# Kernel tuning notes

Hardware: AMD Instinct MI355X
Metric: run time of the kernel (lower is better)

Reference implementation:

```python
import jax, jax.numpy as jnp
import numpy as np

B, L, C, H, DK, MAXREL = 4, 1024, 768, 12, 64, 7
NEG = -2.0 ** 15  # masked_fill value


def _rel_pos_table(L, m):
    # abs distance, compressed logarithmically beyond m, clipped to [0, 2m]
    i = jnp.arange(L, dtype=jnp.float32)
    d = jnp.abs(i[:, None] - i[None, :])
    comp = m + jnp.log2(jnp.maximum(d - m, 1.0))
    d = jnp.where(d > m, comp, d)
    return jnp.clip(d, 0, 2 * m).astype(jnp.int32)  # [L, L]


def setup_inputs() -> dict:
    key = jax.random.key(0)
    ks = jax.random.split(key, 16)
    s = 0.02
    return {
        "qx": jax.random.normal(ks[0], (B, L, C), jnp.float32),
        "kx": jax.random.normal(ks[1], (B, L, C), jnp.float32),
        "vx": jax.random.normal(ks[2], (B, L, C), jnp.float32),
        "WQ_w": jax.random.normal(ks[3], (C, H * DK), jnp.float32) * s,
        "WQ_b": jnp.zeros((H * DK,), jnp.float32),
        "WK_w": jax.random.normal(ks[4], (C, H * DK), jnp.float32) * s,
        "WK_b": jnp.zeros((H * DK,), jnp.float32),
        "WV_w": jax.random.normal(ks[5], (C, H * DK), jnp.float32) * s,
        "WV_b": jnp.zeros((H * DK,), jnp.float32),
        "WO_w": jax.random.normal(ks[6], (H * DK, C), jnp.float32) * s,
        "WO_b": jnp.zeros((C,), jnp.float32),
        "embK": jax.random.normal(ks[7], (2 * MAXREL + 1, H), jnp.float32),
        "embB": jax.random.normal(ks[8], (2 * MAXREL + 1, H), jnp.float32) * s,
        "preScores": jax.random.normal(ks[9], (B, H, L, L), jnp.float32) * 0.1,
        "maskPAD": jnp.ones((B, L, L), jnp.int32),
    }


def reference(qx, kx, vx, WQ_w, WQ_b, WK_w, WK_b, WV_w, WV_b, WO_w, WO_b,
              embK, embB, preScores, maskPAD):
    q = (qx @ WQ_w + WQ_b).reshape(B, L, H, DK).transpose(0, 2, 1, 3)  # [B,H,L,dk]
    k = (kx @ WK_w + WK_b).reshape(B, L, H, DK).transpose(0, 2, 1, 3)
    v = (vx @ WV_w + WV_b).reshape(B, L, H, DK).transpose(0, 2, 1, 3)

    scores = jnp.einsum('bhid,bhjd->bhij', q, k) / np.sqrt(DK).astype(np.float32)

    tab = _rel_pos_table(L, MAXREL)                 # [L, L] int
    relK = jnp.transpose(embK[tab], (2, 1, 0))      # [H, L, L] (torch transpose(0,-1))
    relB = jnp.transpose(embB[tab], (2, 1, 0))
    scores = scores * relK[None] + relB[None]

    scores = scores + preScores
    scores = jnp.where((maskPAD == 0)[:, None, :, :], jnp.float32(NEG), scores)

    alpha = jax.nn.softmax(scores, axis=-1)         # dropout is identity in eval
    z = jnp.einsum('bhij,bhjd->bhid', alpha, v)     # [B,H,L,dk]
    z = z.transpose(0, 2, 1, 3).reshape(B, L, H * DK)
    z = z @ WO_w + WO_b
    return (z, scores)
```

## Files before the change

### kernel.cpp

```cpp
#include <hip/hip_runtime.h>
#include <stdint.h>


typedef __attribute__((ext_vector_type(4))) float f32x4;
typedef __attribute__((ext_vector_type(4))) int   i32x4;
typedef __attribute__((ext_vector_type(8))) short short8;
typedef __attribute__((ext_vector_type(4))) unsigned int u32x4;
typedef __attribute__((ext_vector_type(2))) unsigned int u32x2;

__device__ __forceinline__ unsigned short f2bf(float f) {
  unsigned int u = __float_as_uint(f);
  u += 0x7fffu + ((u >> 16) & 1u);
  return (unsigned short)(u >> 16);
}

__global__ __launch_bounds__(256) void conv_x_kernel(
    const float* __restrict__ qx, const float* __restrict__ kx,
    const float* __restrict__ vx, unsigned short* __restrict__ out) {
  int v = blockIdx.x * 256 + threadIdx.x;
  int mat = v / 786432;
  int r = v - mat * 786432;
  const float* src = (mat == 0) ? qx : (mat == 1) ? kx : vx;
  f32x4 x = ((const f32x4*)src)[r];
  union { unsigned short s[4]; u32x2 u; } o;
  o.s[0] = f2bf(x[0]); o.s[1] = f2bf(x[1]); o.s[2] = f2bf(x[2]); o.s[3] = f2bf(x[3]);
  ((u32x2*)out)[v] = o.u;
}

__global__ __launch_bounds__(256) void conv_w_kernel(
    const float* __restrict__ w0, const float* __restrict__ w1,
    const float* __restrict__ w2, const float* __restrict__ w3,
    unsigned short* __restrict__ out) {
  __shared__ float T[64][65];
  int bx = blockIdx.x;
  int mat = bx / 144; int t2 = bx - mat * 144;
  int kt = t2 / 12, nt = t2 - kt * 12;
  int k0 = kt * 64, n0 = nt * 64;
  const float* W = (mat == 0) ? w0 : (mat == 1) ? w1 : (mat == 2) ? w2 : w3;
  unsigned short* WT = out + (size_t)mat * 589824;
  int t = threadIdx.x;
  int lr = t >> 4;
  int lc = (t & 15) * 4;
#pragma unroll
  for (int p = 0; p < 4; p++) {
    int row = p * 16 + lr;
    f32x4 x = *(const f32x4*)&W[(size_t)(k0 + row) * 768 + n0 + lc];
    T[lc + 0][row] = x[0]; T[lc + 1][row] = x[1];
    T[lc + 2][row] = x[2]; T[lc + 3][row] = x[3];
  }
  __syncthreads();
#pragma unroll
  for (int p = 0; p < 4; p++) {
    int row = p * 16 + lr;
    union { unsigned short s[4]; u32x2 u; } o;
    o.s[0] = f2bf(T[row][lc + 0]); o.s[1] = f2bf(T[row][lc + 1]);
    o.s[2] = f2bf(T[row][lc + 2]); o.s[3] = f2bf(T[row][lc + 3]);
    *(u32x2*)&WT[(size_t)(n0 + row) * 768 + k0 + lc] = o.u;
  }
}

__global__ __launch_bounds__(256) void qkv_gemm_kernel(
    const unsigned short* __restrict__ xbf, const unsigned short* __restrict__ wt,
    const float* __restrict__ bq, const float* __restrict__ bk, const float* __restrict__ bv,
    unsigned short* __restrict__ qo, unsigned short* __restrict__ ko,
    unsigned short* __restrict__ vto) {
  __shared__ unsigned short As[128 * 72];
  __shared__ unsigned short Bs[128 * 72];
  int bx = blockIdx.x;
  int mat = bx / 192; int rem = bx - mat * 192;
  int mt = rem / 6, nt = rem - mt * 6;
  int m0 = mt * 128, n0 = nt * 128;
  const unsigned short* A = xbf + (size_t)mat * 4096 * 768;
  const unsigned short* Bm = wt + (size_t)mat * 768 * 768;
  int t = threadIdx.x;
  int wave = t >> 6, lane = t & 63;
  int wm = (wave >> 1) * 64, wn = (wave & 1) * 64;
  int col = lane & 15, quad = lane >> 4;
  int srow = t >> 3;
  int sch = (t & 7) * 8;

  f32x4 acc[4][4];
#pragma unroll
  for (int i = 0; i < 4; i++)
#pragma unroll
    for (int j = 0; j < 4; j++) acc[i][j] = (f32x4){0.f, 0.f, 0.f, 0.f};

  for (int kk = 0; kk < 768; kk += 64) {
#pragma unroll
    for (int p = 0; p < 4; p++) {
      int row = srow + p * 32;
      *(u32x4*)&As[row * 72 + sch] = *(const u32x4*)&A[(size_t)(m0 + row) * 768 + kk + sch];
      *(u32x4*)&Bs[row * 72 + sch] = *(const u32x4*)&Bm[(size_t)(n0 + row) * 768 + kk + sch];
    }
    __syncthreads();
#pragma unroll
    for (int c = 0; c < 2; c++) {
      short8 af[4], bf[4];
#pragma unroll
      for (int i = 0; i < 4; i++) {
        af[i] = *(const short8*)&As[(wm + i * 16 + col) * 72 + c * 32 + quad * 8];
        bf[i] = *(const short8*)&Bs[(wn + i * 16 + col) * 72 + c * 32 + quad * 8];
      }
#pragma unroll
      for (int i = 0; i < 4; i++)
#pragma unroll
        for (int j = 0; j < 4; j++)
          acc[i][j] = __builtin_amdgcn_mfma_f32_16x16x32_bf16(af[i], bf[j], acc[i][j], 0, 0, 0);
    }
    __syncthreads();
  }
  const float* bias = (mat == 0) ? bq : (mat == 1) ? bk : bv;
#pragma unroll
  for (int j = 0; j < 4; j++) {
    int gn = n0 + wn + j * 16 + col;
    float bsv = bias[gn];
    int h = gn >> 6, d = gn & 63;
#pragma unroll
    for (int i = 0; i < 4; i++) {
#pragma unroll
      for (int r = 0; r < 4; r++) {
        int gm = m0 + wm + i * 16 + quad * 4 + r;
        int b = gm >> 10, l = gm & 1023;
        unsigned short v = f2bf(acc[i][j][r] + bsv);
        if (mat == 0)      qo[((size_t)(b * 12 + h) * 1024 + l) * 64 + d] = v;
        else if (mat == 1) ko[((size_t)(b * 12 + h) * 1024 + l) * 64 + d] = v;
        else               vto[((size_t)(b * 12 + h) * 64 + d) * 1024 + l] = v;
      }
    }
  }
}

__global__ __launch_bounds__(256) void attn_kernel(
    const unsigned short* __restrict__ q, const unsigned short* __restrict__ k,
    const unsigned short* __restrict__ vt, const float* __restrict__ preS,
    const int* __restrict__ maskP, const float* __restrict__ embK,
    const float* __restrict__ embB, float* __restrict__ scores,
    unsigned short* __restrict__ zpre) {
  __shared__ unsigned short Qs[64 * 72];
  __shared__ unsigned short Ks[64 * 72];
  __shared__ unsigned short Vs[64 * 72];
  __shared__ unsigned short Ps[64 * 72];
  __shared__ float eK[16], eB[16];
  int bx = blockIdx.x;
  int slice = bx % 48, it = bx / 48;
  int b = slice / 12, h = slice - b * 12;
  int i0 = it * 64;
  int t = threadIdx.x, wave = t >> 6, lane = t & 63;
  int col = lane & 15, quad = lane >> 4;
  int srow = t >> 3, sch = (t & 7) * 8;

  if (t < 15) { eK[t] = embK[t * 12 + h]; eB[t] = embB[t * 12 + h]; }

  const unsigned short* qbase = q + ((size_t)(b * 12 + h) * 1024 + i0) * 64;
#pragma unroll
  for (int p = 0; p < 2; p++) {
    int row = srow + p * 32;
    *(u32x4*)&Qs[row * 72 + sch] = *(const u32x4*)&qbase[(size_t)row * 64 + sch];
  }
  __syncthreads();
  short8 qf[2];
  qf[0] = *(const short8*)&Qs[(wave * 16 + col) * 72 + quad * 8];
  qf[1] = *(const short8*)&Qs[(wave * 16 + col) * 72 + 32 + quad * 8];

  f32x4 oacc[4];
#pragma unroll
  for (int nd = 0; nd < 4; nd++) oacc[nd] = (f32x4){0.f, 0.f, 0.f, 0.f};
  float m_s = -3.0e38f, l_s = 0.f;

  const unsigned short* kbase = k + (size_t)(b * 12 + h) * 1024 * 64;
  const unsigned short* vbase = vt + (size_t)(b * 12 + h) * 64 * 1024;
  const float* pbase = preS + ((size_t)(b * 12 + h) * 1024 + i0) * 1024;
  const int* mbase = maskP + ((size_t)b * 1024 + i0) * 1024;
  float* sbase = scores + ((size_t)(b * 12 + h) * 1024 + i0) * 1024;
  int lrow = wave * 16 + col;
  int gi = i0 + lrow;

  for (int jt = 0; jt < 16; jt++) {
    int j0 = jt * 64;
#pragma unroll
    for (int p = 0; p < 2; p++) {
      int row = srow + p * 32;
      *(u32x4*)&Ks[row * 72 + sch] = *(const u32x4*)&kbase[(size_t)(j0 + row) * 64 + sch];
      *(u32x4*)&Vs[row * 72 + sch] = *(const u32x4*)&vbase[(size_t)row * 1024 + j0 + sch];
    }
    __syncthreads();

    f32x4 sacc[4];
#pragma unroll
    for (int ns = 0; ns < 4; ns++) sacc[ns] = (f32x4){0.f, 0.f, 0.f, 0.f};
#pragma unroll
    for (int c = 0; c < 2; c++) {
#pragma unroll
      for (int ns = 0; ns < 4; ns++) {
        short8 kf = *(const short8*)&Ks[(ns * 16 + col) * 72 + c * 32 + quad * 8];
        sacc[ns] = __builtin_amdgcn_mfma_f32_16x16x32_bf16(kf, qf[c], sacc[ns], 0, 0, 0);
      }
    }

    float sv[4][4];
#pragma unroll
    for (int ns = 0; ns < 4; ns++) {
      int gj0 = j0 + ns * 16 + quad * 4;
      f32x4 pre = *(const f32x4*)&pbase[(size_t)lrow * 1024 + gj0];
      i32x4 mk = *(const i32x4*)&mbase[(size_t)lrow * 1024 + gj0];
      f32x4 sout;
#pragma unroll
      for (int r = 0; r < 4; r++) {
        int dd = gi - (gj0 + r); dd = dd < 0 ? -dd : dd;
        int idx;
        if (dd <= 7) idx = dd;
        else { idx = 38 - __clz(dd - 7); idx = idx > 14 ? 14 : idx; }
        float s = sacc[ns][r] * 0.125f * eK[idx] + eB[idx] + pre[r];
        if (mk[r] == 0) s = -32768.0f;
        sout[r] = s; sv[ns][r] = s;
      }
      *(f32x4*)&sbase[(size_t)lrow * 1024 + gj0] = sout;
    }

    float mx = sv[0][0];
#pragma unroll
    for (int ns = 0; ns < 4; ns++)
#pragma unroll
      for (int r = 0; r < 4; r++) mx = fmaxf(mx, sv[ns][r]);
    mx = fmaxf(mx, __shfl_xor(mx, 16));
    mx = fmaxf(mx, __shfl_xor(mx, 32));
    float mn = fmaxf(m_s, mx);
    float alpha = __expf(m_s - mn);
    float rs = 0.f;
#pragma unroll
    for (int ns = 0; ns < 4; ns++)
#pragma unroll
      for (int r = 0; r < 4; r++) { float p = __expf(sv[ns][r] - mn); sv[ns][r] = p; rs += p; }
    rs += __shfl_xor(rs, 16); rs += __shfl_xor(rs, 32);
    l_s = l_s * alpha + rs;
    m_s = mn;
#pragma unroll
    for (int nd = 0; nd < 4; nd++)
#pragma unroll
      for (int r = 0; r < 4; r++) oacc[nd][r] *= alpha;

#pragma unroll
    for (int ns = 0; ns < 4; ns++) {
      union { unsigned short s[4]; u32x2 u; } pk;
#pragma unroll
      for (int r = 0; r < 4; r++) pk.s[r] = f2bf(sv[ns][r]);
      *(u32x2*)&Ps[(size_t)lrow * 72 + ns * 16 + quad * 4] = pk.u;
    }

#pragma unroll
    for (int c2 = 0; c2 < 2; c2++) {
      short8 pf = *(const short8*)&Ps[(wave * 16 + col) * 72 + c2 * 32 + quad * 8];
#pragma unroll
      for (int nd = 0; nd < 4; nd++) {
        short8 vf = *(const short8*)&Vs[(nd * 16 + col) * 72 + c2 * 32 + quad * 8];
        oacc[nd] = __builtin_amdgcn_mfma_f32_16x16x32_bf16(vf, pf, oacc[nd], 0, 0, 0);
      }
    }
    __syncthreads();
  }

  float inv = 1.0f / fmaxf(l_s, 1e-30f);
  unsigned short* zb = zpre + ((size_t)(b * 12 + h) * 1024 + i0 + lrow) * 64;
#pragma unroll
  for (int nd = 0; nd < 4; nd++) {
    union { unsigned short s[4]; u32x2 u; } zk;
#pragma unroll
    for (int r = 0; r < 4; r++) zk.s[r] = f2bf(oacc[nd][r] * inv);
    *(u32x2*)&zb[nd * 16 + quad * 4] = zk.u;
  }
}

__global__ __launch_bounds__(256) void out_gemm_kernel(
    const unsigned short* __restrict__ zpre, const unsigned short* __restrict__ wot,
    const float* __restrict__ wob, float* __restrict__ zout) {
  __shared__ unsigned short As[128 * 72];
  __shared__ unsigned short Bs[128 * 72];
  int bx = blockIdx.x;
  int mt = bx / 6, nt = bx - mt * 6;
  int m0 = mt * 128, n0 = nt * 128;
  int t = threadIdx.x;
  int wave = t >> 6, lane = t & 63;
  int wm = (wave >> 1) * 64, wn = (wave & 1) * 64;
  int col = lane & 15, quad = lane >> 4;
  int srow = t >> 3, sch = (t & 7) * 8;

  f32x4 acc[4][4];
#pragma unroll
  for (int i = 0; i < 4; i++)
#pragma unroll
    for (int j = 0; j < 4; j++) acc[i][j] = (f32x4){0.f, 0.f, 0.f, 0.f};

  for (int kk = 0; kk < 768; kk += 64) {
    int hh = kk >> 6;
#pragma unroll
    for (int p = 0; p < 4; p++) {
      int row = srow + p * 32;
      int gm = m0 + row;
      int b = gm >> 10, l = gm & 1023;
      *(u32x4*)&As[row * 72 + sch] =
          *(const u32x4*)&zpre[((size_t)(b * 12 + hh) * 1024 + l) * 64 + sch];
      *(u32x4*)&Bs[row * 72 + sch] = *(const u32x4*)&wot[(size_t)(n0 + row) * 768 + kk + sch];
    }
    __syncthreads();
#pragma unroll
    for (int c = 0; c < 2; c++) {
      short8 af[4], bf[4];
#pragma unroll
      for (int i = 0; i < 4; i++) {
        af[i] = *(const short8*)&As[(wm + i * 16 + col) * 72 + c * 32 + quad * 8];
        bf[i] = *(const short8*)&Bs[(wn + i * 16 + col) * 72 + c * 32 + quad * 8];
      }
#pragma unroll
      for (int i = 0; i < 4; i++)
#pragma unroll
        for (int j = 0; j < 4; j++)
          acc[i][j] = __builtin_amdgcn_mfma_f32_16x16x32_bf16(af[i], bf[j], acc[i][j], 0, 0, 0);
    }
    __syncthreads();
  }
#pragma unroll
  for (int j = 0; j < 4; j++) {
    int gn = n0 + wn + j * 16 + col;
    float bsv = wob[gn];
#pragma unroll
    for (int i = 0; i < 4; i++) {
#pragma unroll
      for (int r = 0; r < 4; r++) {
        int gm = m0 + wm + i * 16 + quad * 4 + r;
        zout[(size_t)gm * 768 + gn] = acc[i][j][r] + bsv;
      }
    }
  }
}

extern "C" void kernel_launch(void* const* d_in, const int* in_sizes, int n_in,
                              void* d_out, int out_size, void* d_ws, size_t ws_size,
                              hipStream_t stream) {
  const float* qx   = (const float*)d_in[0];
  const float* kx   = (const float*)d_in[1];
  const float* vx   = (const float*)d_in[2];
  const float* WQ_w = (const float*)d_in[3];
  const float* WQ_b = (const float*)d_in[4];
  const float* WK_w = (const float*)d_in[5];
  const float* WK_b = (const float*)d_in[6];
  const float* WV_w = (const float*)d_in[7];
  const float* WV_b = (const float*)d_in[8];
  const float* WO_w = (const float*)d_in[9];
  const float* WO_b = (const float*)d_in[10];
  const float* embK = (const float*)d_in[11];
  const float* embB = (const float*)d_in[12];
  const float* preS = (const float*)d_in[13];
  const int* maskP  = (const int*)d_in[14];

  float* zout = (float*)d_out;
  float* scores = zout + 3145728;
  unsigned short* xbf = (unsigned short*)scores;

  char* ws = (char*)d_ws;
  unsigned short* wt  = (unsigned short*)(ws);
  unsigned short* qb  = (unsigned short*)(ws + 4718592);
  unsigned short* kb  = (unsigned short*)(ws + 11010048);
  unsigned short* vtb = (unsigned short*)(ws + 17301504);
  unsigned short* zp  = (unsigned short*)(ws + 23592960);

  conv_x_kernel<<<9216, 256, 0, stream>>>(qx, kx, vx, xbf);
  conv_w_kernel<<<576, 256, 0, stream>>>(WQ_w, WK_w, WV_w, WO_w, wt);
  qkv_gemm_kernel<<<576, 256, 0, stream>>>(xbf, wt, WQ_b, WK_b, WV_b, qb, kb, vtb);
  attn_kernel<<<768, 256, 0, stream>>>(qb, kb, vtb, preS, maskP, embK, embB, scores, zp);
  out_gemm_kernel<<<192, 256, 0, stream>>>(zp, wt + 3 * 589824, WO_b, zout);
}
```

Baseline: 520.8 us.

## Double-buffer shared tiles and register-prefetch in QKV, attention and output GEMM kernels

Adds register-staged prefetching with double-buffered LDS tiles to the QKV GEMM, attention and output GEMM loops, so global loads for the next tiles overlap MFMA compute and one barrier per iteration is removed. The attention kernel also prefetches preScores one tile ahead and K/V two tiles ahead, reusing the Q buffer as the P buffer. The V output is now transposed through LDS for coalesced stores. The output GEMM drops to 64x64 tiles with four times as many blocks. Register pressure and launch-bound occupancy hints may limit the overlap.

```diff
diff --git a/kernel.cpp b/kernel.cpp
--- a/kernel.cpp
+++ b/kernel.cpp
@@ -59,13 +59,12 @@
   }
 }
 
-__global__ __launch_bounds__(256) void qkv_gemm_kernel(
+__global__ __launch_bounds__(256, 2) void qkv_gemm_kernel(
     const unsigned short* __restrict__ xbf, const unsigned short* __restrict__ wt,
     const float* __restrict__ bq, const float* __restrict__ bk, const float* __restrict__ bv,
     unsigned short* __restrict__ qo, unsigned short* __restrict__ ko,
     unsigned short* __restrict__ vto) {
-  __shared__ unsigned short As[128 * 72];
-  __shared__ unsigned short Bs[128 * 72];
+  __shared__ unsigned short SM[2][2][128 * 72];
   int bx = blockIdx.x;
   int mat = bx / 192; int rem = bx - mat * 192;
   int mt = rem / 6, nt = rem - mt * 6;
@@ -85,14 +84,27 @@
 #pragma unroll
     for (int j = 0; j < 4; j++) acc[i][j] = (f32x4){0.f, 0.f, 0.f, 0.f};
 
-  for (int kk = 0; kk < 768; kk += 64) {
-#pragma unroll
-    for (int p = 0; p < 4; p++) {
-      int row = srow + p * 32;
-      *(u32x4*)&As[row * 72 + sch] = *(const u32x4*)&A[(size_t)(m0 + row) * 768 + kk + sch];
-      *(u32x4*)&Bs[row * 72 + sch] = *(const u32x4*)&Bm[(size_t)(n0 + row) * 768 + kk + sch];
-    }
-    __syncthreads();
+  u32x4 ra[4], rb[4];
+#pragma unroll
+  for (int p = 0; p < 4; p++) {
+    ra[p] = *(const u32x4*)&A[(size_t)(m0 + srow + p * 32) * 768 + sch];
+    rb[p] = *(const u32x4*)&Bm[(size_t)(n0 + srow + p * 32) * 768 + sch];
+  }
+#pragma unroll
+  for (int p = 0; p < 4; p++) {
+    *(u32x4*)&SM[0][0][(srow + p * 32) * 72 + sch] = ra[p];
+    *(u32x4*)&SM[0][1][(srow + p * 32) * 72 + sch] = rb[p];
+  }
+#pragma unroll
+  for (int p = 0; p < 4; p++) {
+    ra[p] = *(const u32x4*)&A[(size_t)(m0 + srow + p * 32) * 768 + 64 + sch];
+    rb[p] = *(const u32x4*)&Bm[(size_t)(n0 + srow + p * 32) * 768 + 64 + sch];
+  }
+  __syncthreads();
+
+  for (int it = 0; it < 12; ++it) {
+    const unsigned short* As = SM[it & 1][0];
+    const unsigned short* Bs = SM[it & 1][1];
 #pragma unroll
     for (int c = 0; c < 2; c++) {
       short8 af[4], bf[4];
@@ -107,40 +119,188 @@
         for (int j = 0; j < 4; j++)
           acc[i][j] = __builtin_amdgcn_mfma_f32_16x16x32_bf16(af[i], bf[j], acc[i][j], 0, 0, 0);
     }
+    if (it < 11) {
+      unsigned short* An = SM[(it + 1) & 1][0];
+      unsigned short* Bn = SM[(it + 1) & 1][1];
+#pragma unroll
+      for (int p = 0; p < 4; p++) {
+        *(u32x4*)&An[(srow + p * 32) * 72 + sch] = ra[p];
+        *(u32x4*)&Bn[(srow + p * 32) * 72 + sch] = rb[p];
+      }
+      if (it < 10) {
+        int kk2 = (it + 2) * 64;
+#pragma unroll
+        for (int p = 0; p < 4; p++) {
+          ra[p] = *(const u32x4*)&A[(size_t)(m0 + srow + p * 32) * 768 + kk2 + sch];
+          rb[p] = *(const u32x4*)&Bm[(size_t)(n0 + srow + p * 32) * 768 + kk2 + sch];
+        }
+      }
+      __syncthreads();
+    }
+  }
+
+  if (mat != 2) {
+    const float* bias = (mat == 0) ? bq : bk;
+    unsigned short* dst = (mat == 0) ? qo : ko;
+#pragma unroll
+    for (int j = 0; j < 4; j++) {
+      int gn = n0 + wn + j * 16 + col;
+      float bsv = bias[gn];
+      int h = gn >> 6, d = gn & 63;
+#pragma unroll
+      for (int i = 0; i < 4; i++) {
+#pragma unroll
+        for (int r = 0; r < 4; r++) {
+          int gm = m0 + wm + i * 16 + quad * 4 + r;
+          int b = gm >> 10, l = gm & 1023;
+          dst[((size_t)(b * 12 + h) * 1024 + l) * 64 + d] = f2bf(acc[i][j][r] + bsv);
+        }
+      }
+    }
+  } else {
+    unsigned short* Tr = &SM[0][0][0];
     __syncthreads();
-  }
-  const float* bias = (mat == 0) ? bq : (mat == 1) ? bk : bv;
-#pragma unroll
-  for (int j = 0; j < 4; j++) {
-    int gn = n0 + wn + j * 16 + col;
-    float bsv = bias[gn];
-    int h = gn >> 6, d = gn & 63;
-#pragma unroll
-    for (int i = 0; i < 4; i++) {
-#pragma unroll
-      for (int r = 0; r < 4; r++) {
-        int gm = m0 + wm + i * 16 + quad * 4 + r;
-        int b = gm >> 10, l = gm & 1023;
-        unsigned short v = f2bf(acc[i][j][r] + bsv);
-        if (mat == 0)      qo[((size_t)(b * 12 + h) * 1024 + l) * 64 + d] = v;
-        else if (mat == 1) ko[((size_t)(b * 12 + h) * 1024 + l) * 64 + d] = v;
-        else               vto[((size_t)(b * 12 + h) * 64 + d) * 1024 + l] = v;
-      }
-    }
-  }
-}
-
-__global__ __launch_bounds__(256) void attn_kernel(
+#pragma unroll
+    for (int j = 0; j < 4; j++) {
+      int n = wn + j * 16 + col;
+      float bsv = bv[n0 + n];
+#pragma unroll
+      for (int i = 0; i < 4; i++) {
+        int m = wm + i * 16 + quad * 4;
+        union { unsigned short s[4]; u32x2 u; } pk;
+#pragma unroll
+        for (int r = 0; r < 4; r++) pk.s[r] = f2bf(acc[i][j][r] + bsv);
+        *(u32x2*)&Tr[(size_t)n * 132 + m] = pk.u;
+      }
+    }
+    __syncthreads();
+#pragma unroll
+    for (int p = 0; p < 8; p++) {
+      int row = (t >> 4) + p * 16;
+      int ch = (t & 15) * 8;
+      u32x4 val = *(const u32x4*)&Tr[(size_t)row * 132 + ch];
+      int gn = n0 + row;
+      int h = gn >> 6, d = gn & 63;
+      int gm = m0 + ch;
+      int b = gm >> 10, l = gm & 1023;
+      *(u32x4*)&vto[((size_t)(b * 12 + h) * 64 + d) * 1024 + l] = val;
+    }
+  }
+}
+
+struct KV { u32x4 k0, k1, v0, v1; };
+
+__device__ __forceinline__ void attn_body(
+    int jt, const unsigned short* KsC, const unsigned short* VsC,
+    unsigned short* KsN, unsigned short* VsN,
+    f32x4* preC, f32x4* preN, KV& kvW, KV& kvF,
+    const short8* qf, f32x4* oacc, float& m_s, float& l_s,
+    const unsigned short* kbase, const unsigned short* vbase,
+    const float* pbase, const int* mbase, float* sbase,
+    unsigned short* Ps, const float* eK, const float* eB,
+    int lrow, int gi, int srow, int sch, int col, int quad, int wave) {
+  const int j0 = jt * 64;
+  i32x4 mk[4];
+#pragma unroll
+  for (int ns = 0; ns < 4; ns++)
+    mk[ns] = *(const i32x4*)&mbase[(size_t)lrow * 1024 + j0 + ns * 16 + quad * 4];
+  if (jt < 15) {
+    int jp1 = (jt + 1) * 64;
+#pragma unroll
+    for (int ns = 0; ns < 4; ns++)
+      preN[ns] = *(const f32x4*)&pbase[(size_t)lrow * 1024 + jp1 + ns * 16 + quad * 4];
+  }
+  if (jt < 14) {
+    int jp2 = (jt + 2) * 64;
+    kvF.k0 = *(const u32x4*)&kbase[(size_t)(jp2 + srow) * 64 + sch];
+    kvF.k1 = *(const u32x4*)&kbase[(size_t)(jp2 + srow + 32) * 64 + sch];
+    kvF.v0 = *(const u32x4*)&vbase[(size_t)srow * 1024 + jp2 + sch];
+    kvF.v1 = *(const u32x4*)&vbase[(size_t)(srow + 32) * 1024 + jp2 + sch];
+  }
+  f32x4 sacc[4];
+#pragma unroll
+  for (int ns = 0; ns < 4; ns++) sacc[ns] = (f32x4){0.f, 0.f, 0.f, 0.f};
+#pragma unroll
+  for (int c = 0; c < 2; c++) {
+#pragma unroll
+    for (int ns = 0; ns < 4; ns++) {
+      short8 kf = *(const short8*)&KsC[(ns * 16 + col) * 72 + c * 32 + quad * 8];
+      sacc[ns] = __builtin_amdgcn_mfma_f32_16x16x32_bf16(kf, qf[c], sacc[ns], 0, 0, 0);
+    }
+  }
+  float sv[4][4];
+#pragma unroll
+  for (int ns = 0; ns < 4; ns++) {
+    int gj0 = j0 + ns * 16 + quad * 4;
+    f32x4 sout;
+#pragma unroll
+    for (int r = 0; r < 4; r++) {
+      int dd = gi - (gj0 + r); dd = dd < 0 ? -dd : dd;
+      int idx;
+      if (dd <= 7) idx = dd;
+      else { idx = 38 - __clz(dd - 7); idx = idx > 14 ? 14 : idx; }
+      float s = sacc[ns][r] * 0.125f * eK[idx] + eB[idx] + preC[ns][r];
+      if (mk[ns][r] == 0) s = -32768.0f;
+      sout[r] = s; sv[ns][r] = s;
+    }
+    *(f32x4*)&sbase[(size_t)lrow * 1024 + gj0] = sout;
+  }
+  float mx = sv[0][0];
+#pragma unroll
+  for (int ns = 0; ns < 4; ns++)
+#pragma unroll
+    for (int r = 0; r < 4; r++) mx = fmaxf(mx, sv[ns][r]);
+  mx = fmaxf(mx, __shfl_xor(mx, 16));
+  mx = fmaxf(mx, __shfl_xor(mx, 32));
+  float mn = fmaxf(m_s, mx);
+  float alpha = __expf(m_s - mn);
+  float rs = 0.f;
+#pragma unroll
+  for (int ns = 0; ns < 4; ns++)
+#pragma unroll
+    for (int r = 0; r < 4; r++) { float p = __expf(sv[ns][r] - mn); sv[ns][r] = p; rs += p; }
+  rs += __shfl_xor(rs, 16); rs += __shfl_xor(rs, 32);
+  l_s = l_s * alpha + rs;
+  m_s = mn;
+#pragma unroll
+  for (int nd = 0; nd < 4; nd++)
+#pragma unroll
+    for (int r = 0; r < 4; r++) oacc[nd][r] *= alpha;
+#pragma unroll
+  for (int ns = 0; ns < 4; ns++) {
+    union { unsigned short s[4]; u32x2 u; } pk;
+#pragma unroll
+    for (int r = 0; r < 4; r++) pk.s[r] = f2bf(sv[ns][r]);
+    *(u32x2*)&Ps[(size_t)lrow * 72 + ns * 16 + quad * 4] = pk.u;
+  }
+#pragma unroll
+  for (int c2 = 0; c2 < 2; c2++) {
+    short8 pf = *(const short8*)&Ps[(wave * 16 + col) * 72 + c2 * 32 + quad * 8];
+#pragma unroll
+    for (int nd = 0; nd < 4; nd++) {
+      short8 vf = *(const short8*)&VsC[(nd * 16 + col) * 72 + c2 * 32 + quad * 8];
+      oacc[nd] = __builtin_amdgcn_mfma_f32_16x16x32_bf16(vf, pf, oacc[nd], 0, 0, 0);
+    }
+  }
+  if (jt < 15) {
+    *(u32x4*)&KsN[srow * 72 + sch] = kvW.k0;
+    *(u32x4*)&KsN[(srow + 32) * 72 + sch] = kvW.k1;
+    *(u32x4*)&VsN[srow * 72 + sch] = kvW.v0;
+    *(u32x4*)&VsN[(srow + 32) * 72 + sch] = kvW.v1;
+    __syncthreads();
+  }
+}
+
+__global__ __launch_bounds__(256, 3) void attn_kernel(
     const unsigned short* __restrict__ q, const unsigned short* __restrict__ k,
     const unsigned short* __restrict__ vt, const float* __restrict__ preS,
     const int* __restrict__ maskP, const float* __restrict__ embK,
     const float* __restrict__ embB, float* __restrict__ scores,
     unsigned short* __restrict__ zpre) {
   __shared__ unsigned short Qs[64 * 72];
-  __shared__ unsigned short Ks[64 * 72];
-  __shared__ unsigned short Vs[64 * 72];
-  __shared__ unsigned short Ps[64 * 72];
-  __shared__ float eK[16], eB[16];
+  __shared__ unsigned short KsB[2][64 * 72];
+  __shared__ unsigned short VsB[2][64 * 72];
+  __shared__ float eKs[16], eBs[16];
   int bx = blockIdx.x;
   int slice = bx % 48, it = bx / 48;
   int b = slice / 12, h = slice - b * 12;
@@ -149,24 +309,9 @@
   int col = lane & 15, quad = lane >> 4;
   int srow = t >> 3, sch = (t & 7) * 8;
 
-  if (t < 15) { eK[t] = embK[t * 12 + h]; eB[t] = embB[t * 12 + h]; }
+  if (t < 15) { eKs[t] = embK[t * 12 + h]; eBs[t] = embB[t * 12 + h]; }
 
   const unsigned short* qbase = q + ((size_t)(b * 12 + h) * 1024 + i0) * 64;
-#pragma unroll
-  for (int p = 0; p < 2; p++) {
-    int row = srow + p * 32;
-    *(u32x4*)&Qs[row * 72 + sch] = *(const u32x4*)&qbase[(size_t)row * 64 + sch];
-  }
-  __syncthreads();
-  short8 qf[2];
-  qf[0] = *(const short8*)&Qs[(wave * 16 + col) * 72 + quad * 8];
-  qf[1] = *(const short8*)&Qs[(wave * 16 + col) * 72 + 32 + quad * 8];
-
-  f32x4 oacc[4];
-#pragma unroll
-  for (int nd = 0; nd < 4; nd++) oacc[nd] = (f32x4){0.f, 0.f, 0.f, 0.f};
-  float m_s = -3.0e38f, l_s = 0.f;
-
   const unsigned short* kbase = k + (size_t)(b * 12 + h) * 1024 * 64;
   const unsigned short* vbase = vt + (size_t)(b * 12 + h) * 64 * 1024;
   const float* pbase = preS + ((size_t)(b * 12 + h) * 1024 + i0) * 1024;
@@ -175,88 +320,48 @@
   int lrow = wave * 16 + col;
   int gi = i0 + lrow;
 
-  for (int jt = 0; jt < 16; jt++) {
-    int j0 = jt * 64;
-#pragma unroll
-    for (int p = 0; p < 2; p++) {
-      int row = srow + p * 32;
-      *(u32x4*)&Ks[row * 72 + sch] = *(const u32x4*)&kbase[(size_t)(j0 + row) * 64 + sch];
-      *(u32x4*)&Vs[row * 72 + sch] = *(const u32x4*)&vbase[(size_t)row * 1024 + j0 + sch];
-    }
-    __syncthreads();
-
-    f32x4 sacc[4];
-#pragma unroll
-    for (int ns = 0; ns < 4; ns++) sacc[ns] = (f32x4){0.f, 0.f, 0.f, 0.f};
-#pragma unroll
-    for (int c = 0; c < 2; c++) {
-#pragma unroll
-      for (int ns = 0; ns < 4; ns++) {
-        short8 kf = *(const short8*)&Ks[(ns * 16 + col) * 72 + c * 32 + quad * 8];
-        sacc[ns] = __builtin_amdgcn_mfma_f32_16x16x32_bf16(kf, qf[c], sacc[ns], 0, 0, 0);
-      }
-    }
-
-    float sv[4][4];
-#pragma unroll
-    for (int ns = 0; ns < 4; ns++) {
-      int gj0 = j0 + ns * 16 + quad * 4;
-      f32x4 pre = *(const f32x4*)&pbase[(size_t)lrow * 1024 + gj0];
-      i32x4 mk = *(const i32x4*)&mbase[(size_t)lrow * 1024 + gj0];
-      f32x4 sout;
-#pragma unroll
-      for (int r = 0; r < 4; r++) {
-        int dd = gi - (gj0 + r); dd = dd < 0 ? -dd : dd;
-        int idx;
-        if (dd <= 7) idx = dd;
-        else { idx = 38 - __clz(dd - 7); idx = idx > 14 ? 14 : idx; }
-        float s = sacc[ns][r] * 0.125f * eK[idx] + eB[idx] + pre[r];
-        if (mk[r] == 0) s = -32768.0f;
-        sout[r] = s; sv[ns][r] = s;
-      }
-      *(f32x4*)&sbase[(size_t)lrow * 1024 + gj0] = sout;
-    }
-
-    float mx = sv[0][0];
-#pragma unroll
-    for (int ns = 0; ns < 4; ns++)
-#pragma unroll
-      for (int r = 0; r < 4; r++) mx = fmaxf(mx, sv[ns][r]);
-    mx = fmaxf(mx, __shfl_xor(mx, 16));
-    mx = fmaxf(mx, __shfl_xor(mx, 32));
-    float mn = fmaxf(m_s, mx);
-    float alpha = __expf(m_s - mn);
-    float rs = 0.f;
-#pragma unroll
-    for (int ns = 0; ns < 4; ns++)
-#pragma unroll
-      for (int r = 0; r < 4; r++) { float p = __expf(sv[ns][r] - mn); sv[ns][r] = p; rs += p; }
-    rs += __shfl_xor(rs, 16); rs += __shfl_xor(rs, 32);
-    l_s = l_s * alpha + rs;
-    m_s = mn;
-#pragma unroll
-    for (int nd = 0; nd < 4; nd++)
-#pragma unroll
-      for (int r = 0; r < 4; r++) oacc[nd][r] *= alpha;
-
-#pragma unroll
-    for (int ns = 0; ns < 4; ns++) {
-      union { unsigned short s[4]; u32x2 u; } pk;
-#pragma unroll
-      for (int r = 0; r < 4; r++) pk.s[r] = f2bf(sv[ns][r]);
-      *(u32x2*)&Ps[(size_t)lrow * 72 + ns * 16 + quad * 4] = pk.u;
-    }
-
-#pragma unroll
-    for (int c2 = 0; c2 < 2; c2++) {
-      short8 pf = *(const short8*)&Ps[(wave * 16 + col) * 72 + c2 * 32 + quad * 8];
-#pragma unroll
-      for (int nd = 0; nd < 4; nd++) {
-        short8 vf = *(const short8*)&Vs[(nd * 16 + col) * 72 + c2 * 32 + quad * 8];
-        oacc[nd] = __builtin_amdgcn_mfma_f32_16x16x32_bf16(vf, pf, oacc[nd], 0, 0, 0);
-      }
-    }
-    __syncthreads();
+#pragma unroll
+  for (int p = 0; p < 2; p++) {
+    int row = srow + p * 32;
+    *(u32x4*)&Qs[row * 72 + sch] = *(const u32x4*)&qbase[(size_t)row * 64 + sch];
+  }
+  __syncthreads();
+  short8 qf[2];
+  qf[0] = *(const short8*)&Qs[(wave * 16 + col) * 72 + quad * 8];
+  qf[1] = *(const short8*)&Qs[(wave * 16 + col) * 72 + 32 + quad * 8];
+
+  f32x4 oacc[4];
+#pragma unroll
+  for (int nd = 0; nd < 4; nd++) oacc[nd] = (f32x4){0.f, 0.f, 0.f, 0.f};
+  float m_s = -3.0e38f, l_s = 0.f;
+
+  KV kvA, kvB;
+  f32x4 preA[4], preB[4];
+  kvA.k0 = *(const u32x4*)&kbase[(size_t)srow * 64 + sch];
+  kvA.k1 = *(const u32x4*)&kbase[(size_t)(srow + 32) * 64 + sch];
+  kvA.v0 = *(const u32x4*)&vbase[(size_t)srow * 1024 + sch];
+  kvA.v1 = *(const u32x4*)&vbase[(size_t)(srow + 32) * 1024 + sch];
+  *(u32x4*)&KsB[0][srow * 72 + sch] = kvA.k0;
+  *(u32x4*)&KsB[0][(srow + 32) * 72 + sch] = kvA.k1;
+  *(u32x4*)&VsB[0][srow * 72 + sch] = kvA.v0;
+  *(u32x4*)&VsB[0][(srow + 32) * 72 + sch] = kvA.v1;
+#pragma unroll
+  for (int ns = 0; ns < 4; ns++)
+    preA[ns] = *(const f32x4*)&pbase[(size_t)lrow * 1024 + ns * 16 + quad * 4];
+  kvB.k0 = *(const u32x4*)&kbase[(size_t)(64 + srow) * 64 + sch];
+  kvB.k1 = *(const u32x4*)&kbase[(size_t)(64 + srow + 32) * 64 + sch];
+  kvB.v0 = *(const u32x4*)&vbase[(size_t)srow * 1024 + 64 + sch];
+  kvB.v1 = *(const u32x4*)&vbase[(size_t)(srow + 32) * 1024 + 64 + sch];
+  __syncthreads();
+
+  unsigned short* Ps = Qs;
+  for (int jt = 0; jt < 16; jt += 2) {
+    attn_body(jt,     KsB[0], VsB[0], KsB[1], VsB[1], preA, preB, kvB, kvA,
+              qf, oacc, m_s, l_s, kbase, vbase, pbase, mbase, sbase,
+              Ps, eKs, eBs, lrow, gi, srow, sch, col, quad, wave);
+    attn_body(jt + 1, KsB[1], VsB[1], KsB[0], VsB[0], preB, preA, kvA, kvB,
+              qf, oacc, m_s, l_s, kbase, vbase, pbase, mbase, sbase,
+              Ps, eKs, eBs, lrow, gi, srow, sch, col, quad, wave);
   }
 
   float inv = 1.0f / fmaxf(l_s, 1e-30f);
@@ -270,60 +375,83 @@
   }
 }
 
-__global__ __launch_bounds__(256) void out_gemm_kernel(
+__global__ __launch_bounds__(256, 3) void out_gemm_kernel(
     const unsigned short* __restrict__ zpre, const unsigned short* __restrict__ wot,
     const float* __restrict__ wob, float* __restrict__ zout) {
-  __shared__ unsigned short As[128 * 72];
-  __shared__ unsigned short Bs[128 * 72];
+  __shared__ unsigned short SM[2][2][64 * 72];
   int bx = blockIdx.x;
-  int mt = bx / 6, nt = bx - mt * 6;
-  int m0 = mt * 128, n0 = nt * 128;
+  int mt = bx / 12, nt = bx - mt * 12;
+  int m0 = mt * 64, n0 = nt * 64;
   int t = threadIdx.x;
   int wave = t >> 6, lane = t & 63;
-  int wm = (wave >> 1) * 64, wn = (wave & 1) * 64;
+  int wm = (wave >> 1) * 32, wn = (wave & 1) * 32;
   int col = lane & 15, quad = lane >> 4;
   int srow = t >> 3, sch = (t & 7) * 8;
-
-  f32x4 acc[4][4];
-#pragma unroll
-  for (int i = 0; i < 4; i++)
-#pragma unroll
-    for (int j = 0; j < 4; j++) acc[i][j] = (f32x4){0.f, 0.f, 0.f, 0.f};
-
-  for (int kk = 0; kk < 768; kk += 64) {
-    int hh = kk >> 6;
-#pragma unroll
-    for (int p = 0; p < 4; p++) {
-      int row = srow + p * 32;
-      int gm = m0 + row;
-      int b = gm >> 10, l = gm & 1023;
-      *(u32x4*)&As[row * 72 + sch] =
-          *(const u32x4*)&zpre[((size_t)(b * 12 + hh) * 1024 + l) * 64 + sch];
-      *(u32x4*)&Bs[row * 72 + sch] = *(const u32x4*)&wot[(size_t)(n0 + row) * 768 + kk + sch];
-    }
-    __syncthreads();
+  int gmA0 = m0 + srow, gmA1 = m0 + srow + 32;
+  int bA0 = gmA0 >> 10, lA0 = gmA0 & 1023;
+  int bA1 = gmA1 >> 10, lA1 = gmA1 & 1023;
+
+  f32x4 acc[2][2];
+#pragma unroll
+  for (int i = 0; i < 2; i++)
+#pragma unroll
+    for (int j = 0; j < 2; j++) acc[i][j] = (f32x4){0.f, 0.f, 0.f, 0.f};
+
+  u32x4 ra[2], rb[2];
+  ra[0] = *(const u32x4*)&zpre[((size_t)(bA0 * 12 + 0) * 1024 + lA0) * 64 + sch];
+  ra[1] = *(const u32x4*)&zpre[((size_t)(bA1 * 12 + 0) * 1024 + lA1) * 64 + sch];
+  rb[0] = *(const u32x4*)&wot[(size_t)(n0 + srow) * 768 + sch];
+  rb[1] = *(const u32x4*)&wot[(size_t)(n0 + srow + 32) * 768 + sch];
+  *(u32x4*)&SM[0][0][srow * 72 + sch] = ra[0];
+  *(u32x4*)&SM[0][0][(srow + 32) * 72 + sch] = ra[1];
+  *(u32x4*)&SM[0][1][srow * 72 + sch] = rb[0];
+  *(u32x4*)&SM[0][1][(srow + 32) * 72 + sch] = rb[1];
+  ra[0] = *(const u32x4*)&zpre[((size_t)(bA0 * 12 + 1) * 1024 + lA0) * 64 + sch];
+  ra[1] = *(const u32x4*)&zpre[((size_t)(bA1 * 12 + 1) * 1024 + lA1) * 64 + sch];
+  rb[0] = *(const u32x4*)&wot[(size_t)(n0 + srow) * 768 + 64 + sch];
+  rb[1] = *(const u32x4*)&wot[(size_t)(n0 + srow + 32) * 768 + 64 + sch];
+  __syncthreads();
+
+  for (int it = 0; it < 12; ++it) {
+    const unsigned short* As = SM[it & 1][0];
+    const unsigned short* Bs = SM[it & 1][1];
 #pragma unroll
     for (int c = 0; c < 2; c++) {
-      short8 af[4], bf[4];
-#pragma unroll
-      for (int i = 0; i < 4; i++) {
+      short8 af[2], bf[2];
+#pragma unroll
+      for (int i = 0; i < 2; i++) {
         af[i] = *(const short8*)&As[(wm + i * 16 + col) * 72 + c * 32 + quad * 8];
         bf[i] = *(const short8*)&Bs[(wn + i * 16 + col) * 72 + c * 32 + quad * 8];
       }
 #pragma unroll
-      for (int i = 0; i < 4; i++)
-#pragma unroll
-        for (int j = 0; j < 4; j++)
+      for (int i = 0; i < 2; i++)
+#pragma unroll
+        for (int j = 0; j < 2; j++)
           acc[i][j] = __builtin_amdgcn_mfma_f32_16x16x32_bf16(af[i], bf[j], acc[i][j], 0, 0, 0);
     }
-    __syncthreads();
-  }
-#pragma unroll
-  for (int j = 0; j < 4; j++) {
+    if (it < 11) {
+      unsigned short* An = SM[(it + 1) & 1][0];
+      unsigned short* Bn = SM[(it + 1) & 1][1];
+      *(u32x4*)&An[srow * 72 + sch] = ra[0];
+      *(u32x4*)&An[(srow + 32) * 72 + sch] = ra[1];
+      *(u32x4*)&Bn[srow * 72 + sch] = rb[0];
+      *(u32x4*)&Bn[(srow + 32) * 72 + sch] = rb[1];
+      if (it < 10) {
+        int hh = it + 2;
+        ra[0] = *(const u32x4*)&zpre[((size_t)(bA0 * 12 + hh) * 1024 + lA0) * 64 + sch];
+        ra[1] = *(const u32x4*)&zpre[((size_t)(bA1 * 12 + hh) * 1024 + lA1) * 64 + sch];
+        rb[0] = *(const u32x4*)&wot[(size_t)(n0 + srow) * 768 + hh * 64 + sch];
+        rb[1] = *(const u32x4*)&wot[(size_t)(n0 + srow + 32) * 768 + hh * 64 + sch];
+      }
+      __syncthreads();
+    }
+  }
+#pragma unroll
+  for (int j = 0; j < 2; j++) {
     int gn = n0 + wn + j * 16 + col;
     float bsv = wob[gn];
 #pragma unroll
-    for (int i = 0; i < 4; i++) {
+    for (int i = 0; i < 2; i++) {
 #pragma unroll
       for (int r = 0; r < 4; r++) {
         int gm = m0 + wm + i * 16 + quad * 4 + r;
@@ -367,5 +495,5 @@
   conv_w_kernel<<<576, 256, 0, stream>>>(WQ_w, WK_w, WV_w, WO_w, wt);
   qkv_gemm_kernel<<<576, 256, 0, stream>>>(xbf, wt, WQ_b, WK_b, WV_b, qb, kb, vtb);
   attn_kernel<<<768, 256, 0, stream>>>(qb, kb, vtb, preS, maskP, embK, embB, scores, zp);
-  out_gemm_kernel<<<192, 256, 0, stream>>>(zp, wt + 3 * 589824, WO_b, zout);
-}
+  out_gemm_kernel<<<192 * 4, 256, 0, stream>>>(zp, wt + 3 * 589824, WO_b, zout);
+}
```

After: 483.3 us. 1.08x faster.
